# Performance work log

Hardware: AMD Instinct MI355X
Metric: run time of the kernel (lower is better)

## Reference

```python
import jax, jax.numpy as jnp
import numpy as np

B, T = 2, 512
E, NH, HD, V, P, L, KER, BLOCK = 768, 12, 64, 256, 4, 4, 16, 512
SCALE = HD ** -0.5


def _ln(x, g, b, eps=1e-5):
    m = jnp.mean(x, -1, keepdims=True)
    v = jnp.mean((x - m) ** 2, -1, keepdims=True)
    return (x - m) * jax.lax.rsqrt(v + eps) * g + b


def _rope_tables(n):
    inv = 1.0 / (10000.0 ** (jnp.arange(0, HD, 2, dtype=jnp.float32) / HD))
    f = jnp.arange(n, dtype=jnp.float32)[:, None] * inv[None, :]
    return jnp.cos(f), jnp.sin(f)


def _rope(x, cos, sin):
    # rotate over last two dims (positions, HD); split-half RoPE as in source
    h = x.shape[-1] // 2
    x1, x2 = x[..., :h], x[..., h:]
    return jnp.concatenate([x1 * cos - x2 * sin, x1 * sin + x2 * cos], axis=-1)


def _patch_attn(x, qkv_w, S):
    # x: [B,T,E]; sliding-window patch attention, step=1
    Bb, Tt, _ = x.shape
    q, k, v = jnp.split(x @ qkv_w, 3, axis=-1)
    heads = lambda t: t.reshape(Bb, Tt, NH, HD).transpose(0, 2, 1, 3)  # [B,NH,T,HD]
    q, k, v = heads(q), heads(k), heads(v)
    cos, sin = _rope_tables(Tt)
    q = _rope(q, cos, sin)
    k = _rope(k, cos, sin)
    # prefix: full causal attention over first S tokens
    sc = jnp.einsum('bnqh,bnkh->bnqk', q[:, :, :S], k[:, :, :S]) * SCALE
    mask = jnp.tril(jnp.ones((S, S), dtype=bool))
    sc = jnp.where(mask, sc, jnp.float32(-jnp.inf))
    out = jnp.einsum('bnqk,bnkh->bnqh', jax.nn.softmax(sc, axis=-1), v[:, :, :S])
    if Tt > S:
        # query t (t>=S) attends keys [t-S+1, t] (mask_sliding is all-ones for step=1)
        idx = jnp.arange(Tt - S)[:, None] + 1 + jnp.arange(S)[None, :]  # [T-S,S]
        kw = k[:, :, idx]  # [B,NH,T-S,S,HD]
        vw = v[:, :, idx]
        qs = q[:, :, S:]   # [B,NH,T-S,HD]
        sw = jnp.einsum('bnth,bntsh->bnts', qs, kw) * SCALE
        ow = jnp.einsum('bnts,bntsh->bnth', jax.nn.softmax(sw, axis=-1), vw)
        out = jnp.concatenate([out, ow], axis=2)
    return out.transpose(0, 2, 1, 3).reshape(Bb, Tt, NH * HD)


def _sa_block(x, ln0g, ln0b, ln1g, ln1b, qkv_w, proj_w, proj_b, w1, b1, w2, b2):
    # x: [B,T,P,V]; full (unmasked) attention over the P prediction slots
    Bb, Tt, Pp, _ = x.shape
    h = _ln(x, ln0g, ln0b)
    q, k, v = jnp.split(h @ qkv_w, 3, axis=-1)
    heads = lambda t: t.reshape(Bb, Tt, Pp, NH, HD).transpose(0, 1, 3, 2, 4)  # [B,T,NH,P,HD]
    q, k, v = heads(q), heads(k), heads(v)
    cos, sin = _rope_tables(Pp)
    q = _rope(q, cos, sin)
    k = _rope(k, cos, sin)
    sc = jnp.einsum('btnph,btnqh->btnpq', q, k) * SCALE
    o = jnp.einsum('btnpq,btnqh->btnph', jax.nn.softmax(sc, axis=-1), v)
    o = o.transpose(0, 1, 3, 2, 4).reshape(Bb, Tt, Pp, NH * HD)
    x = x + (o @ proj_w + proj_b)
    h2 = _ln(x, ln1g, ln1b)
    ff = jax.nn.gelu(h2 @ w1 + b1, approximate=False) @ w2 + b2
    return x + ff


def _forward(tokens, emb, blk_ln0_g, blk_ln0_b, blk_ln1_g, blk_ln1_b, blk_qkv_w,
             blk_ff_w1, blk_ff_b1, blk_ff_w2, blk_ff_b2, fin_ln_g, fin_ln_b,
             head_w, head_b, sa_ln0_g, sa_ln0_b, sa_ln1_g, sa_ln1_b, sa_qkv_w,
             sa_proj_w, sa_proj_b, sa_ff_w1, sa_ff_b1, sa_ff_w2, sa_ff_b2):
    x0 = emb[tokens]  # [B,T,E]
    x = x0
    for i in range(L):
        S = min(KER * 2 ** i, BLOCK)
        h = _ln(x, blk_ln0_g[i], blk_ln0_b[i])
        x = x + _patch_attn(h, blk_qkv_w[i], S)
        h2 = _ln(x, blk_ln1_g[i], blk_ln1_b[i])
        x = x + (jax.nn.gelu(h2 @ blk_ff_w1[i] + blk_ff_b1[i], approximate=False)
                 @ blk_ff_w2[i] + blk_ff_b2[i])
    x = x0 + x  # Golu: x = token_embedding(x); x = x + blocks(x)
    x = _ln(x, fin_ln_g, fin_ln_b)
    logits = (x @ head_w + head_b).reshape(B, T, P, V)
    logits = _sa_block(logits, sa_ln0_g, sa_ln0_b, sa_ln1_g, sa_ln1_b, sa_qkv_w,
                       sa_proj_w, sa_proj_b, sa_ff_w1, sa_ff_b1, sa_ff_w2, sa_ff_b2)
    return logits[:, :, 0, :]  # [B,T,V] (y is None path)


def setup_inputs() -> dict:
    key = jax.random.key(0)
    ks = jax.random.split(key, 12)
    w = lambda k, sh: jax.random.normal(k, sh, dtype=jnp.float32) * 0.02
    return {
        'tokens': jax.random.randint(ks[0], (B, T), 0, V),
        'emb': w(ks[1], (V, E)),
        'blk_ln0_g': jnp.ones((L, E), jnp.float32),
        'blk_ln0_b': jnp.zeros((L, E), jnp.float32),
        'blk_ln1_g': jnp.ones((L, E), jnp.float32),
        'blk_ln1_b': jnp.zeros((L, E), jnp.float32),
        'blk_qkv_w': w(ks[2], (L, E, 3 * E)),
        'blk_ff_w1': w(ks[3], (L, E, 4 * E)),
        'blk_ff_b1': jnp.zeros((L, 4 * E), jnp.float32),
        'blk_ff_w2': w(ks[4], (L, 4 * E, E)),
        'blk_ff_b2': jnp.zeros((L, E), jnp.float32),
        'fin_ln_g': jnp.ones((E,), jnp.float32),
        'fin_ln_b': jnp.zeros((E,), jnp.float32),
        'head_w': w(ks[5], (E, V * P)),
        'head_b': jnp.zeros((V * P,), jnp.float32),
        'sa_ln0_g': jnp.ones((V,), jnp.float32),
        'sa_ln0_b': jnp.zeros((V,), jnp.float32),
        'sa_ln1_g': jnp.ones((V,), jnp.float32),
        'sa_ln1_b': jnp.zeros((V,), jnp.float32),
        'sa_qkv_w': w(ks[6], (V, 3 * E)),
        'sa_proj_w': w(ks[7], (E, V)),
        'sa_proj_b': jnp.zeros((V,), jnp.float32),
        'sa_ff_w1': w(ks[8], (V, 4 * V)),
        'sa_ff_b1': jnp.zeros((4 * V,), jnp.float32),
        'sa_ff_w2': w(ks[9], (4 * V, V)),
        'sa_ff_b2': jnp.zeros((V,), jnp.float32),
    }


def reference(tokens, emb, blk_ln0_g, blk_ln0_b, blk_ln1_g, blk_ln1_b, blk_qkv_w,
              blk_ff_w1, blk_ff_b1, blk_ff_w2, blk_ff_b2, fin_ln_g, fin_ln_b,
              head_w, head_b, sa_ln0_g, sa_ln0_b, sa_ln1_g, sa_ln1_b, sa_qkv_w,
              sa_proj_w, sa_proj_b, sa_ff_w1, sa_ff_b1, sa_ff_w2, sa_ff_b2):
    return _forward(tokens, emb, blk_ln0_g, blk_ln0_b, blk_ln1_g, blk_ln1_b,
                    blk_qkv_w, blk_ff_w1, blk_ff_b1, blk_ff_w2, blk_ff_b2,
                    fin_ln_g, fin_ln_b, head_w, head_b, sa_ln0_g, sa_ln0_b,
                    sa_ln1_g, sa_ln1_b, sa_qkv_w, sa_proj_w, sa_proj_b,
                    sa_ff_w1, sa_ff_b1, sa_ff_w2, sa_ff_b2)
```

## Files before the change

kernel.cpp:

```cpp
#include <hip/hip_runtime.h>
#include <hip/hip_bf16.h>
#include <cstdint>
#include <cstddef>

#define BB    2
#define TSEQ  512
#define EDIM  768
#define NHEAD 12
#define HDIM  64
#define VDIM  256
#define PDIM  4
#define NROW  (BB*TSEQ)
#define NROW2 (BB*TSEQ*PDIM)

typedef __attribute__((ext_vector_type(8))) short short8;
typedef __attribute__((ext_vector_type(4))) short short4v;
typedef __attribute__((ext_vector_type(4))) float floatx4;

__device__ __forceinline__ float gelu_f(float v){
    return 0.5f * v * (1.0f + erff(v * 0.70710678118654752f));
}
__device__ __forceinline__ float b2f(short s){
    unsigned u = ((unsigned)(unsigned short)s) << 16;
    float f; __builtin_memcpy(&f, &u, 4); return f;
}
__device__ __forceinline__ short f2bs(float v){
    __hip_bfloat16 h = __float2bfloat16(v);
    short s; __builtin_memcpy(&s, &h, 2); return s;
}
__device__ __forceinline__ void gload16(const void* g, void* l){
    __builtin_amdgcn_global_load_lds((const __attribute__((address_space(1))) void*)g,
                                     (__attribute__((address_space(3))) void*)l, 16, 0, 0);
}

#define WAITN(n) asm volatile("s_waitcnt vmcnt(" #n ")" ::: "memory")
#define WAIT_STAGE(rem, full, half)                         \
    do{ if((rem) >= 2)      WAITN(full);                    \
        else if((rem) == 1) WAITN(half);                    \
        else                WAITN(0);                       \
        asm volatile("s_barrier" ::: "memory"); }while(0)

struct WD2 { const float* in; __hip_bfloat16* out; int K; int N; int nt; };
struct WDs { WD2 d[17]; };

__global__ __launch_bounds__(256) void wconv_all(WDs a)
{
    int id = blockIdx.x;
    int i = 0;
    while(i < 16 && id >= a.d[i].nt){ id -= a.d[i].nt; i++; }
    WD2 w = a.d[i];
    const int tx = w.N / 128;
    const int n0 = (id % tx) * 128, k0 = (id / tx) * 128;
    __shared__ short t[128*128];
    {
        const int c4 = (threadIdx.x & 31) * 4;
        const int r0 = threadIdx.x >> 5;
        #pragma unroll
        for(int half = 0; half < 2; half++){
            float4 v[8];
            #pragma unroll
            for(int it = 0; it < 8; it++){
                int r = r0 + it*8 + half*64;
                v[it] = *(const float4*)(w.in + (size_t)(k0 + r) * w.N + n0 + c4);
            }
            #pragma unroll
            for(int it = 0; it < 8; it++){
                int r = r0 + it*8 + half*64;
                int nswz = c4 ^ (((r >> 3) & 15) << 2);
                short4v o;
                o[0] = f2bs(v[it].x); o[1] = f2bs(v[it].y);
                o[2] = f2bs(v[it].z); o[3] = f2bs(v[it].w);
                *(short4v*)&t[r*128 + nswz] = o;
            }
        }
    }
    __syncthreads();
    {
        const int k8 = (threadIdx.x & 15) * 8;
        const int nr = threadIdx.x >> 4;
        const int swz = (k8 >> 3) << 2;
        #pragma unroll
        for(int pass = 0; pass < 8; pass++){
            int n = nr + pass*16;
            int nswz = n ^ swz;
            short8 o;
            #pragma unroll
            for(int j = 0; j < 8; j++) o[j] = t[(k8 + j)*128 + nswz];
            *(short8*)((short*)w.out + (size_t)(n0 + n) * w.K + k0 + k8) = o;
        }
    }
}

template<int ACT, int RESID, int OUTBF16, int ROPESA>
__global__ __launch_bounds__(256) void gemm128(
    const short* __restrict__ A, const short* __restrict__ Bt,
    const float* __restrict__ bias, const float* __restrict__ resid,
    void* __restrict__ Cout, const float* __restrict__ rc, const float* __restrict__ rs,
    int M, int N, int K)
{
    alignas(16) __shared__ short As[4*128*32];
    alignas(16) __shared__ short Bs[4*128*32];
    const int tid  = threadIdx.x;
    const int lane = tid & 63;
    const int wave = tid >> 6;
    const int bm = blockIdx.y * 128, bn = blockIdx.x * 128;
    const int wm = (wave >> 1) * 64, wn = (wave & 1) * 64;
    const int quad = lane >> 4, l16 = lane & 15;

    floatx4 acc[4][4];
    #pragma unroll
    for(int i = 0; i < 4; i++)
        #pragma unroll
        for(int j = 0; j < 4; j++)
            acc[i][j] = floatx4{0.f, 0.f, 0.f, 0.f};

    const int r  = tid >> 2;
    const int c8 = (tid & 3) * 8;
    const int ldsoff = (tid & 192) * 16;

    auto issue = [&](int k0, int cur){
        char* ab = (char*)As + cur*8192 + ldsoff;
        char* bb = (char*)Bs + cur*8192 + ldsoff;
        gload16(A  + (size_t)(bm + r     ) * K + k0 + c8, ab);
        gload16(A  + (size_t)(bm + r + 64) * K + k0 + c8, ab + 4096);
        gload16(Bt + (size_t)(bn + r     ) * K + k0 + c8, bb);
        gload16(Bt + (size_t)(bn + r + 64) * K + k0 + c8, bb + 4096);
    };

    const int niter = K >> 5;
    issue(0, 0); issue(32, 1); issue(64, 2);
    for(int it = 0; it < niter; it++){
        WAIT_STAGE(niter - 1 - it, 8, 4);
        if(it + 3 < niter) issue((it + 3) << 5, (it + 3) & 3);
        const short* Ab = As + (it & 3) * 4096;
        const short* Bb = Bs + (it & 3) * 4096;
        short8 af[4], bfr[4];
        #pragma unroll
        for(int i = 0; i < 4; i++){
            af[i]  = *(const short8*)&Ab[(wm + i*16 + l16)*32 + quad*8];
            bfr[i] = *(const short8*)&Bb[(wn + i*16 + l16)*32 + quad*8];
        }
        #pragma unroll
        for(int i = 0; i < 4; i++)
            #pragma unroll
            for(int j = 0; j < 4; j++)
                acc[i][j] = __builtin_amdgcn_mfma_f32_16x16x32_bf16(af[i], bfr[j], acc[i][j], 0, 0, 0);
    }

    float* Cf = (float*)Cout;
    __hip_bfloat16* Cb = (__hip_bfloat16*)Cout;

    if(ROPESA){
        const int hb = bn + wn;
        const int region = hb / 768;
        #pragma unroll
        for(int i = 0; i < 4; i++){
            #pragma unroll
            for(int rr = 0; rr < 4; rr++){
                int row = bm + wm + i*16 + quad*4 + rr;
                float a0 = acc[i][0][rr], a1 = acc[i][1][rr];
                float a2 = acc[i][2][rr], a3 = acc[i][3][rr];
                size_t rowb = (size_t)row * N + hb;
                if(region == 2){
                    Cb[rowb + l16]      = __float2bfloat16(a0);
                    Cb[rowb + 16 + l16] = __float2bfloat16(a1);
                    Cb[rowb + 32 + l16] = __float2bfloat16(a2);
                    Cb[rowb + 48 + l16] = __float2bfloat16(a3);
                }else{
                    int p = row & 3;
                    float c0 = rc[p*32 + l16],      s0 = rs[p*32 + l16];
                    float c1 = rc[p*32 + 16 + l16], s1 = rs[p*32 + 16 + l16];
                    Cb[rowb + l16]      = __float2bfloat16(a0*c0 - a2*s0);
                    Cb[rowb + 16 + l16] = __float2bfloat16(a1*c1 - a3*s1);
                    Cb[rowb + 32 + l16] = __float2bfloat16(a0*s0 + a2*c0);
                    Cb[rowb + 48 + l16] = __float2bfloat16(a1*s1 + a3*c1);
                }
            }
        }
        return;
    }

    #pragma unroll
    for(int i = 0; i < 4; i++){
        int row0 = bm + wm + i*16 + quad*4;
        #pragma unroll
        for(int j = 0; j < 4; j++){
            int col = bn + wn + j*16 + l16;
            float bv = bias ? bias[col] : 0.f;
            #pragma unroll
            for(int rr = 0; rr < 4; rr++){
                float v = acc[i][j][rr] + bv;
                if(ACT) v = gelu_f(v);
                if(RESID) v += resid[(size_t)(row0 + rr) * N + col];
                if(OUTBF16) Cb[(size_t)(row0 + rr) * N + col] = __float2bfloat16(v);
                else        Cf[(size_t)(row0 + rr) * N + col] = v;
            }
        }
    }
}

template<int EPI>
__global__ __launch_bounds__(256) void gemm64q(
    const short* __restrict__ A, const short* __restrict__ Bt,
    const float* __restrict__ bias, __hip_bfloat16* __restrict__ Cout,
    __hip_bfloat16* __restrict__ qrb, __hip_bfloat16* __restrict__ krb,
    __hip_bfloat16* __restrict__ vvb,
    const float* __restrict__ rc, const float* __restrict__ rs,
    int M, int N, int K)
{
    alignas(16) __shared__ short As[4*64*32];
    alignas(16) __shared__ short Bs[4*64*32];
    const int tid  = threadIdx.x;
    const int lane = tid & 63;
    const int wave = tid >> 6;
    const int bm = blockIdx.y * 64, bn = blockIdx.x * 64;
    const int wm = wave * 16;
    const int quad = lane >> 4, l16 = lane & 15;

    floatx4 acc[4];
    #pragma unroll
    for(int j = 0; j < 4; j++) acc[j] = floatx4{0.f, 0.f, 0.f, 0.f};

    const int r  = tid >> 2;
    const int c8 = (tid & 3) * 8;
    const int ldsoff = (tid & 192) * 16;

    auto issue = [&](int k0, int cur){
        char* ab = (char*)As + cur*4096 + ldsoff;
        char* bb = (char*)Bs + cur*4096 + ldsoff;
        gload16(A  + (size_t)(bm + r) * K + k0 + c8, ab);
        gload16(Bt + (size_t)(bn + r) * K + k0 + c8, bb);
    };

    const int niter = K >> 5;
    issue(0, 0); issue(32, 1); issue(64, 2);
    for(int it = 0; it < niter; it++){
        WAIT_STAGE(niter - 1 - it, 4, 2);
        if(it + 3 < niter) issue((it + 3) << 5, (it + 3) & 3);
        const short* Ab = As + (it & 3) * 2048;
        const short* Bb = Bs + (it & 3) * 2048;
        short8 af = *(const short8*)&Ab[(wm + l16)*32 + quad*8];
        short8 bfr[4];
        #pragma unroll
        for(int j = 0; j < 4; j++)
            bfr[j] = *(const short8*)&Bb[(j*16 + l16)*32 + quad*8];
        #pragma unroll
        for(int j = 0; j < 4; j++)
            acc[j] = __builtin_amdgcn_mfma_f32_16x16x32_bf16(af, bfr[j], acc[j], 0, 0, 0);
    }

    if(EPI == 2){
        const int region = bn / 768;
        const int h = (bn % 768) >> 6;
        #pragma unroll
        for(int rr = 0; rr < 4; rr++){
            int row = bm + wm + quad*4 + rr;
            int t = row & (TSEQ-1), b = row >> 9;
            float a0 = acc[0][rr], a1 = acc[1][rr];
            float a2 = acc[2][rr], a3 = acc[3][rr];
            size_t dbase = ((size_t)(b*NHEAD + h)*TSEQ + t)*HDIM;
            if(region == 2){
                vvb[dbase + l16]      = __float2bfloat16(a0);
                vvb[dbase + 16 + l16] = __float2bfloat16(a1);
                vvb[dbase + 32 + l16] = __float2bfloat16(a2);
                vvb[dbase + 48 + l16] = __float2bfloat16(a3);
            }else{
                float c0 = rc[t*32 + l16],      s0 = rs[t*32 + l16];
                float c1 = rc[t*32 + 16 + l16], s1 = rs[t*32 + 16 + l16];
                __hip_bfloat16* dst = (region == 0) ? qrb : krb;
                dst[dbase + l16]      = __float2bfloat16(a0*c0 - a2*s0);
                dst[dbase + 16 + l16] = __float2bfloat16(a1*c1 - a3*s1);
                dst[dbase + 32 + l16] = __float2bfloat16(a0*s0 + a2*c0);
                dst[dbase + 48 + l16] = __float2bfloat16(a1*s1 + a3*c1);
            }
        }
        return;
    }

    if(EPI == 3){
        const int region = bn / 768;
        #pragma unroll
        for(int rr = 0; rr < 4; rr++){
            int row = bm + wm + quad*4 + rr;
            float a0 = acc[0][rr], a1 = acc[1][rr];
            float a2 = acc[2][rr], a3 = acc[3][rr];
            size_t rowb = (size_t)row * N + bn;
            if(region == 2){
                Cout[rowb + l16]      = __float2bfloat16(a0);
                Cout[rowb + 16 + l16] = __float2bfloat16(a1);
                Cout[rowb + 32 + l16] = __float2bfloat16(a2);
                Cout[rowb + 48 + l16] = __float2bfloat16(a3);
            }else{
                int p = row & 3;
                float c0 = rc[p*32 + l16],      s0 = rs[p*32 + l16];
                float c1 = rc[p*32 + 16 + l16], s1 = rs[p*32 + 16 + l16];
                Cout[rowb + l16]      = __float2bfloat16(a0*c0 - a2*s0);
                Cout[rowb + 16 + l16] = __float2bfloat16(a1*c1 - a3*s1);
                Cout[rowb + 32 + l16] = __float2bfloat16(a0*s0 + a2*c0);
                Cout[rowb + 48 + l16] = __float2bfloat16(a1*s1 + a3*c1);
            }
        }
        return;
    }

    #pragma unroll
    for(int j = 0; j < 4; j++){
        int col = bn + j*16 + l16;
        float bv = bias ? bias[col] : 0.f;
        #pragma unroll
        for(int rr = 0; rr < 4; rr++){
            int row = bm + wm + quad*4 + rr;
            float v = acc[j][rr] + bv;
            v = gelu_f(v);
            Cout[(size_t)row * N + col] = __float2bfloat16(v);
        }
    }
}

template<int RESID, int OUTC>
__global__ __launch_bounds__(256) void gemm64t(
    const short* __restrict__ A, const short* __restrict__ Bt,
    const float* __restrict__ bias, const float* __restrict__ resid,
    float* __restrict__ Cf, float* __restrict__ outp, int M, int N, int K)
{
    alignas(16) __shared__ short As[4*64*32];
    alignas(16) __shared__ short Bs[4*64*32];
    const int tid  = threadIdx.x;
    const int lane = tid & 63;
    const int wave = tid >> 6;
    const int bm = blockIdx.y * 64, bn = blockIdx.x * 64;
    const int wm = (wave >> 1) * 32, wn = (wave & 1) * 32;
    const int quad = lane >> 4, l16 = lane & 15;

    floatx4 acc[2][2];
    #pragma unroll
    for(int i = 0; i < 2; i++)
        #pragma unroll
        for(int j = 0; j < 2; j++)
            acc[i][j] = floatx4{0.f, 0.f, 0.f, 0.f};

    const int r  = tid >> 2;
    const int c8 = (tid & 3) * 8;
    const int ldsoff = (tid & 192) * 16;

    auto issue = [&](int k0, int cur){
        char* ab = (char*)As + cur*4096 + ldsoff;
        char* bb = (char*)Bs + cur*4096 + ldsoff;
        gload16(A  + (size_t)(bm + r) * K + k0 + c8, ab);
        gload16(Bt + (size_t)(bn + r) * K + k0 + c8, bb);
    };

    const int niter = K >> 5;
    issue(0, 0); issue(32, 1); issue(64, 2);
    for(int it = 0; it < niter; it++){
        WAIT_STAGE(niter - 1 - it, 4, 2);
        if(it + 3 < niter) issue((it + 3) << 5, (it + 3) & 3);
        const short* Ab = As + (it & 3) * 2048;
        const short* Bb = Bs + (it & 3) * 2048;
        short8 af[2], bfr[2];
        #pragma unroll
        for(int i = 0; i < 2; i++){
            af[i]  = *(const short8*)&Ab[(wm + i*16 + l16)*32 + quad*8];
            bfr[i] = *(const short8*)&Bb[(wn + i*16 + l16)*32 + quad*8];
        }
        #pragma unroll
        for(int i = 0; i < 2; i++)
            #pragma unroll
            for(int j = 0; j < 2; j++)
                acc[i][j] = __builtin_amdgcn_mfma_f32_16x16x32_bf16(af[i], bfr[j], acc[i][j], 0, 0, 0);
    }

    #pragma unroll
    for(int i = 0; i < 2; i++){
        int row0 = bm + wm + i*16 + quad*4;
        #pragma unroll
        for(int j = 0; j < 2; j++){
            int col = bn + wn + j*16 + l16;
            float bv = bias ? bias[col] : 0.f;
            #pragma unroll
            for(int rr = 0; rr < 4; rr++){
                int row = row0 + rr;
                float v = acc[i][j][rr] + bv;
                if(RESID) v += resid[(size_t)row * N + col];
                Cf[(size_t)row * N + col] = v;
                if(OUTC && (row & 3) == 0)
                    outp[(size_t)(row >> 2) * N + col] = v;
            }
        }
    }
}

template<int D>
__global__ __launch_bounds__(256) void ln_wave(
    const float* __restrict__ in, const float* __restrict__ in2,
    const float* __restrict__ g, const float* __restrict__ bta,
    __hip_bfloat16* __restrict__ out)
{
    constexpr int NC = D / 256;
    const int row  = blockIdx.x * 4 + (threadIdx.x >> 6);
    const int lane = threadIdx.x & 63;
    const float* xr = in + (size_t)row * D;
    float4 v[NC];
    float sum = 0.f, sq = 0.f;
    #pragma unroll
    for(int j = 0; j < NC; j++){
        int d0 = (lane + 64*j) * 4;
        v[j] = *(const float4*)(xr + d0);
        if(in2){
            float4 u = *(const float4*)(in2 + (size_t)row * D + d0);
            v[j].x += u.x; v[j].y += u.y; v[j].z += u.z; v[j].w += u.w;
        }
        sum += v[j].x + v[j].y + v[j].z + v[j].w;
        sq  += v[j].x*v[j].x + v[j].y*v[j].y + v[j].z*v[j].z + v[j].w*v[j].w;
    }
    #pragma unroll
    for(int off = 32; off > 0; off >>= 1){
        sum += __shfl_xor(sum, off, 64);
        sq  += __shfl_xor(sq,  off, 64);
    }
    const float m    = sum / D;
    const float rstd = rsqrtf(fmaxf(sq / D - m*m, 0.f) + 1e-5f);
    #pragma unroll
    for(int j = 0; j < NC; j++){
        int d0 = (lane + 64*j) * 4;
        float4 gg = *(const float4*)(g + d0);
        float4 bb = *(const float4*)(bta + d0);
        short4v o;
        o[0] = f2bs((v[j].x - m) * rstd * gg.x + bb.x);
        o[1] = f2bs((v[j].y - m) * rstd * gg.y + bb.y);
        o[2] = f2bs((v[j].z - m) * rstd * gg.z + bb.z);
        o[3] = f2bs((v[j].w - m) * rstd * gg.w + bb.w);
        *(short4v*)((short*)out + (size_t)row * D + d0) = o;
    }
}

__global__ __launch_bounds__(256) void embed_rope(
    const int* __restrict__ tokens, const float* __restrict__ emb,
    float* __restrict__ x0, float* __restrict__ x,
    float* __restrict__ rc, float* __restrict__ rs)
{
    const int blk = blockIdx.x;
    if(blk < NROW){
        const int tok = tokens[blk];
        const float4* src = (const float4*)(emb + (size_t)tok * EDIM);
        float4* d0 = (float4*)(x0 + (size_t)blk * EDIM);
        float4* d1 = (float4*)(x  + (size_t)blk * EDIM);
        if(threadIdx.x < EDIM/4){
            float4 v = src[threadIdx.x]; d0[threadIdx.x] = v; d1[threadIdx.x] = v;
        }
        return;
    }
    int i = (blk - NROW) * 256 + threadIdx.x;
    int pos = i >> 5, d = i & 31;
    float inv = powf(10000.0f, -(float)(2*d) / 64.0f);
    float f = (float)pos * inv;
    rc[i] = cosf(f);
    rs[i] = sinf(f);
}

template<int S>
__global__ __launch_bounds__(256) void patch_attn16(
    const __hip_bfloat16* __restrict__ qr, const __hip_bfloat16* __restrict__ kr,
    const __hip_bfloat16* __restrict__ vv, float* __restrict__ x)
{
    constexpr int W = S + 15;
    alignas(16) __shared__ short Ks[W*64];
    alignas(16) __shared__ short Vs[W*64];
    __shared__ float qlds[16*64];
    __shared__ float pb[16*128];

    const int t0 = blockIdx.x * 16;
    const int h = blockIdx.y, b = blockIdx.z;
    const int tid = threadIdx.x;
    const int wv = tid >> 6, lane = tid & 63;
    const size_t headbase = ((size_t)(b*NHEAD + h)) * TSEQ;

    const int c = tid & 7;
    for(int r = tid >> 3; r < W; r += 32){
        int g = t0 - S + 1 + r;
        int gc = g < 0 ? 0 : g;
        int sc = (c ^ (r & 7)) * 8;
        *(short8*)&Ks[r*64 + sc] = *(const short8*)((const short*)kr + (headbase + gc)*64 + c*8);
        *(short8*)&Vs[r*64 + sc] = *(const short8*)((const short*)vv + (headbase + gc)*64 + c*8);
    }
    for(int i = tid; i < 16*64; i += 256)
        qlds[i] = __bfloat162float(qr[(headbase + t0 + (i >> 6))*64 + (i & 63)]);
    __syncthreads();

    #pragma unroll
    for(int qq = 0; qq < 4; qq++){
        const int ql = wv*4 + qq;
        const int t  = t0 + ql;
        const int r0 = (S >= 64) ? (ql + lane) : ((lane < S) ? (ql + lane) : 0);
        const int r1 = ql + lane + 64;
        float a0 = 0.f, a1 = 0.f;
        #pragma unroll
        for(int ch = 0; ch < 8; ch++){
            float4 qa = *(const float4*)&qlds[ql*64 + ch*8];
            float4 qb = *(const float4*)&qlds[ql*64 + ch*8 + 4];
            short8 k0 = *(const short8*)&Ks[r0*64 + ((ch ^ (r0 & 7))*8)];
            a0 += qa.x*b2f(k0[0]) + qa.y*b2f(k0[1]) + qa.z*b2f(k0[2]) + qa.w*b2f(k0[3])
                + qb.x*b2f(k0[4]) + qb.y*b2f(k0[5]) + qb.z*b2f(k0[6]) + qb.w*b2f(k0[7]);
            if(S == 128){
                short8 k1 = *(const short8*)&Ks[r1*64 + ((ch ^ (r1 & 7))*8)];
                a1 += qa.x*b2f(k1[0]) + qa.y*b2f(k1[1]) + qa.z*b2f(k1[2]) + qa.w*b2f(k1[3])
                    + qb.x*b2f(k1[4]) + qb.y*b2f(k1[5]) + qb.z*b2f(k1[6]) + qb.w*b2f(k1[7]);
            }
        }
        const int key0 = t - S + 1 + lane;
        const bool v0 = (lane < S) && (key0 >= 0);
        const bool v1 = (S == 128) && (key0 + 64 >= 0);
        float s0 = v0 ? a0 * 0.125f : -1e30f;
        float s1 = v1 ? a1 * 0.125f : -1e30f;
        float mx = fmaxf(s0, s1);
        #pragma unroll
        for(int off = 32; off > 0; off >>= 1) mx = fmaxf(mx, __shfl_xor(mx, off, 64));
        float p0 = v0 ? expf(s0 - mx) : 0.f;
        float p1 = v1 ? expf(s1 - mx) : 0.f;
        float sm = p0 + p1;
        #pragma unroll
        for(int off = 32; off > 0; off >>= 1) sm += __shfl_xor(sm, off, 64);
        const float inv = 1.f / sm;
        pb[ql*128 + lane] = p0 * inv;
        if(S == 128) pb[ql*128 + lane + 64] = p1 * inv;
    }

    const int d = lane;
    const int coff = d >> 3, dlo = d & 7;
    #pragma unroll
    for(int qq = 0; qq < 4; qq++){
        const int ql = wv*4 + qq;
        float o = 0.f;
        #pragma unroll 8
        for(int j = 0; j < S; j++){
            int r = ql + j;
            float p = pb[ql*128 + j];
            o += p * b2f(Vs[r*64 + ((coff ^ (r & 7))*8) + dlo]);
        }
        x[((size_t)(b*TSEQ) + t0 + ql) * EDIM + h*HDIM + d] += o;
    }
}

__global__ __launch_bounds__(256) void sa_attn(
    const __hip_bfloat16* __restrict__ qkv2, __hip_bfloat16* __restrict__ o)
{
    const int t = blockIdx.x, h = blockIdx.y, b = blockIdx.z;
    const int p = threadIdx.x >> 6, lane = threadIdx.x & 63;
    const int row0 = (b*TSEQ + t) * PDIM;
    const short* base = (const short*)qkv2 + (size_t)row0 * (3*EDIM);
    const int d = lane;
    float q = b2f(base[(size_t)p*(3*EDIM) + h*HDIM + d]);
    float sc[4];
    #pragma unroll
    for(int j = 0; j < 4; j++){
        float kj = b2f(base[(size_t)j*(3*EDIM) + EDIM + h*HDIM + d]);
        float v = q * kj;
        #pragma unroll
        for(int off = 32; off > 0; off >>= 1) v += __shfl_xor(v, off, 64);
        sc[j] = v * 0.125f;
    }
    float m = fmaxf(fmaxf(sc[0], sc[1]), fmaxf(sc[2], sc[3]));
    float e0 = expf(sc[0]-m), e1 = expf(sc[1]-m), e2 = expf(sc[2]-m), e3 = expf(sc[3]-m);
    float idn = 1.f / (e0 + e1 + e2 + e3);
    float ov = (e0 * b2f(base[0*(3*EDIM) + 2*EDIM + h*HDIM + d])
              + e1 * b2f(base[1*(3*EDIM) + 2*EDIM + h*HDIM + d])
              + e2 * b2f(base[2*(3*EDIM) + 2*EDIM + h*HDIM + d])
              + e3 * b2f(base[3*(3*EDIM) + 2*EDIM + h*HDIM + d])) * idn;
    o[(size_t)(row0 + p) * EDIM + h*HDIM + d] = __float2bfloat16(ov);
}

extern "C" void kernel_launch(void* const* d_in, const int* in_sizes, int n_in,
                              void* d_out, int out_size, void* d_ws, size_t ws_size,
                              hipStream_t stream)
{
    const int*   tokens    = (const int*)  d_in[0];
    const float* emb       = (const float*)d_in[1];
    const float* bl0g      = (const float*)d_in[2];
    const float* bl0b      = (const float*)d_in[3];
    const float* bl1g      = (const float*)d_in[4];
    const float* bl1b      = (const float*)d_in[5];
    const float* qkv_w     = (const float*)d_in[6];
    const float* ff_w1     = (const float*)d_in[7];
    const float* ff_b1     = (const float*)d_in[8];
    const float* ff_w2     = (const float*)d_in[9];
    const float* ff_b2     = (const float*)d_in[10];
    const float* fin_g     = (const float*)d_in[11];
    const float* fin_b     = (const float*)d_in[12];
    const float* head_w    = (const float*)d_in[13];
    const float* head_b    = (const float*)d_in[14];
    const float* sa_ln0_g  = (const float*)d_in[15];
    const float* sa_ln0_b  = (const float*)d_in[16];
    const float* sa_ln1_g  = (const float*)d_in[17];
    const float* sa_ln1_b  = (const float*)d_in[18];
    const float* sa_qkv_w  = (const float*)d_in[19];
    const float* sa_proj_w = (const float*)d_in[20];
    const float* sa_proj_b = (const float*)d_in[21];
    const float* sa_ff_w1  = (const float*)d_in[22];
    const float* sa_ff_b1  = (const float*)d_in[23];
    const float* sa_ff_w2  = (const float*)d_in[24];
    const float* sa_ff_b2  = (const float*)d_in[25];
    float* out = (float*)d_out;

    char* p = (char*)d_ws;
    auto alloc = [&](size_t bytes){ char* q = p; p += (bytes + 255) & ~(size_t)255; return q; };

    float* logits = (float*)alloc((size_t)NROW2*VDIM*4);
    float* ropec  = (float*)alloc(512*32*4);
    float* ropes  = (float*)alloc(512*32*4);
    __hip_bfloat16* wqkvT[4]; for(int i=0;i<4;i++) wqkvT[i] = (__hip_bfloat16*)alloc((size_t)768*2304*2);
    __hip_bfloat16* wff1T[4]; for(int i=0;i<4;i++) wff1T[i] = (__hip_bfloat16*)alloc((size_t)768*3072*2);
    __hip_bfloat16* wff2T[4]; for(int i=0;i<4;i++) wff2T[i] = (__hip_bfloat16*)alloc((size_t)3072*768*2);
    __hip_bfloat16* wheadT   = (__hip_bfloat16*)alloc((size_t)768*1024*2);
    __hip_bfloat16* wsaqkvT  = (__hip_bfloat16*)alloc((size_t)256*2304*2);
    __hip_bfloat16* wsaprojT = (__hip_bfloat16*)alloc((size_t)768*256*2);
    __hip_bfloat16* wsaff1T  = (__hip_bfloat16*)alloc((size_t)256*1024*2);
    __hip_bfloat16* wsaff2T  = (__hip_bfloat16*)alloc((size_t)1024*256*2);
    char* U = p;
    float* x0           = (float*)(U);
    float* x            = (float*)(U + 3145728);
    __hip_bfloat16* h   = (__hip_bfloat16*)(U + 6291456);
    __hip_bfloat16* ff1 = (__hip_bfloat16*)(U + 7864320);
    __hip_bfloat16* qrb = (__hip_bfloat16*)(U + 14155776);
    __hip_bfloat16* krb = (__hip_bfloat16*)(U + 15728640);
    __hip_bfloat16* vvb = (__hip_bfloat16*)(U + 17301504);
    __hip_bfloat16* h2    = (__hip_bfloat16*)(U);
    __hip_bfloat16* qkv2  = (__hip_bfloat16*)(U + 2097152);
    __hip_bfloat16* sa_o  = (__hip_bfloat16*)(U + 20971520);
    __hip_bfloat16* sa_f1 = (__hip_bfloat16*)(U + 27262976);

    embed_rope<<<NROW + 64, 256, 0, stream>>>(tokens, emb, x0, x, ropec, ropes);
    {
        WDs wds; int tot = 0, n = 0;
        auto add = [&](const float* in, __hip_bfloat16* o2, int K, int N){
            wds.d[n++] = WD2{in, o2, K, N, (N/128)*(K/128)};
            tot += (N/128)*(K/128);
        };
        for(int i=0;i<4;i++){
            add(qkv_w + (size_t)i*768*2304, wqkvT[i], 768, 2304);
            add(ff_w1 + (size_t)i*768*3072, wff1T[i], 768, 3072);
            add(ff_w2 + (size_t)i*3072*768, wff2T[i], 3072, 768);
        }
        add(head_w,    wheadT,   768, 1024);
        add(sa_qkv_w,  wsaqkvT,  256, 2304);
        add(sa_proj_w, wsaprojT, 768, 256);
        add(sa_ff_w1,  wsaff1T,  256, 1024);
        add(sa_ff_w2,  wsaff2T, 1024, 256);
        wconv_all<<<tot, 256, 0, stream>>>(wds);
    }

    for(int i = 0; i < 4; i++){
        ln_wave<EDIM><<<NROW/4, 256, 0, stream>>>(x, nullptr, bl0g + i*EDIM, bl0b + i*EDIM, h);
        gemm64q<2><<<dim3(36, 16), 256, 0, stream>>>(
            (const short*)h, (const short*)wqkvT[i], nullptr, nullptr,
            qrb, krb, vvb, ropec, ropes, NROW, 3*EDIM, EDIM);
        dim3 agrid(TSEQ/16, NHEAD, BB);
        if(i == 0)      patch_attn16<16><<<agrid, 256, 0, stream>>>(qrb, krb, vvb, x);
        else if(i == 1) patch_attn16<32><<<agrid, 256, 0, stream>>>(qrb, krb, vvb, x);
        else if(i == 2) patch_attn16<64><<<agrid, 256, 0, stream>>>(qrb, krb, vvb, x);
        else            patch_attn16<128><<<agrid, 256, 0, stream>>>(qrb, krb, vvb, x);
        ln_wave<EDIM><<<NROW/4, 256, 0, stream>>>(x, nullptr, bl1g + i*EDIM, bl1b + i*EDIM, h);
        gemm64q<1><<<dim3(48, 16), 256, 0, stream>>>(
            (const short*)h, (const short*)wff1T[i], ff_b1 + (size_t)i*4*EDIM, ff1,
            nullptr, nullptr, nullptr, nullptr, nullptr, NROW, 4*EDIM, EDIM);
        gemm64t<1,0><<<dim3(12, 16), 256, 0, stream>>>(
            (const short*)ff1, (const short*)wff2T[i], ff_b2 + (size_t)i*EDIM, x, x, nullptr,
            NROW, EDIM, 4*EDIM);
    }

    ln_wave<EDIM><<<NROW/4, 256, 0, stream>>>(x, x0, fin_g, fin_b, h);
    gemm64t<0,0><<<dim3(16, 16), 256, 0, stream>>>(
        (const short*)h, (const short*)wheadT, head_b, nullptr, logits, nullptr,
        NROW, PDIM*VDIM, EDIM);

    ln_wave<VDIM><<<NROW2/4, 256, 0, stream>>>(logits, nullptr, sa_ln0_g, sa_ln0_b, h2);
    gemm64q<3><<<dim3(36, 64), 256, 0, stream>>>(
        (const short*)h2, (const short*)wsaqkvT, nullptr, qkv2,
        nullptr, nullptr, nullptr, ropec, ropes, NROW2, 3*EDIM, VDIM);
    sa_attn<<<dim3(TSEQ, NHEAD, BB), 256, 0, stream>>>(qkv2, sa_o);
    gemm64t<1,0><<<dim3(4, 64), 256, 0, stream>>>(
        (const short*)sa_o, (const short*)wsaprojT, sa_proj_b, logits, logits, nullptr,
        NROW2, VDIM, EDIM);
    ln_wave<VDIM><<<NROW2/4, 256, 0, stream>>>(logits, nullptr, sa_ln1_g, sa_ln1_b, h2);
    gemm64q<1><<<dim3(16, 64), 256, 0, stream>>>(
        (const short*)h2, (const short*)wsaff1T, sa_ff_b1, sa_f1,
        nullptr, nullptr, nullptr, nullptr, nullptr, NROW2, 4*VDIM, VDIM);
    gemm64t<1,1><<<dim3(4, 64), 256, 0, stream>>>(
        (const short*)sa_f1, (const short*)wsaff2T, sa_ff_b2, logits, logits, out,
        NROW2, VDIM, 4*VDIM);
}
```

Measured before the change: 667.1 us.

## Replace 64x64 fp32-output GEMM with 32x64 two-wave kernel and 8-stage pipeline

Replaces the 64x64-tile, 4-wave gemm64t with gemm32t, which uses a 32x64 tile, two waves (each owning 16 rows across all 64 columns) and an 8-deep global-to-LDS prefetch ring in place of 4. The smaller tile doubles the grid for the narrow-N GEMMs (FF2, head, SA proj, SA FF2), aiming to fill more CUs. The deeper prefetch is meant to hide memory latency for the long-K FF2. In exchange, B tiles are reloaded by twice as many blocks and each wave does less MFMA work per LDS read. The unused gemm128 kernel is also deleted.

```diff
diff --git a/kernel.cpp b/kernel.cpp
--- a/kernel.cpp
+++ b/kernel.cpp
@@ -37,6 +37,15 @@
 #define WAIT_STAGE(rem, full, half)                         \
     do{ if((rem) >= 2)      WAITN(full);                    \
         else if((rem) == 1) WAITN(half);                    \
+        else                WAITN(0);                       \
+        asm volatile("s_barrier" ::: "memory"); }while(0)
+#define WAIT_STAGE8(rem)                                    \
+    do{ if((rem) >= 6)      WAITN(18);                      \
+        else if((rem) == 5) WAITN(15);                      \
+        else if((rem) == 4) WAITN(12);                      \
+        else if((rem) == 3) WAITN(9);                       \
+        else if((rem) == 2) WAITN(6);                       \
+        else if((rem) == 1) WAITN(3);                       \
         else                WAITN(0);                       \
         asm volatile("s_barrier" ::: "memory"); }while(0)
 
@@ -87,114 +96,6 @@
             #pragma unroll
             for(int j = 0; j < 8; j++) o[j] = t[(k8 + j)*128 + nswz];
             *(short8*)((short*)w.out + (size_t)(n0 + n) * w.K + k0 + k8) = o;
-        }
-    }
-}
-
-template<int ACT, int RESID, int OUTBF16, int ROPESA>
-__global__ __launch_bounds__(256) void gemm128(
-    const short* __restrict__ A, const short* __restrict__ Bt,
-    const float* __restrict__ bias, const float* __restrict__ resid,
-    void* __restrict__ Cout, const float* __restrict__ rc, const float* __restrict__ rs,
-    int M, int N, int K)
-{
-    alignas(16) __shared__ short As[4*128*32];
-    alignas(16) __shared__ short Bs[4*128*32];
-    const int tid  = threadIdx.x;
-    const int lane = tid & 63;
-    const int wave = tid >> 6;
-    const int bm = blockIdx.y * 128, bn = blockIdx.x * 128;
-    const int wm = (wave >> 1) * 64, wn = (wave & 1) * 64;
-    const int quad = lane >> 4, l16 = lane & 15;
-
-    floatx4 acc[4][4];
-    #pragma unroll
-    for(int i = 0; i < 4; i++)
-        #pragma unroll
-        for(int j = 0; j < 4; j++)
-            acc[i][j] = floatx4{0.f, 0.f, 0.f, 0.f};
-
-    const int r  = tid >> 2;
-    const int c8 = (tid & 3) * 8;
-    const int ldsoff = (tid & 192) * 16;
-
-    auto issue = [&](int k0, int cur){
-        char* ab = (char*)As + cur*8192 + ldsoff;
-        char* bb = (char*)Bs + cur*8192 + ldsoff;
-        gload16(A  + (size_t)(bm + r     ) * K + k0 + c8, ab);
-        gload16(A  + (size_t)(bm + r + 64) * K + k0 + c8, ab + 4096);
-        gload16(Bt + (size_t)(bn + r     ) * K + k0 + c8, bb);
-        gload16(Bt + (size_t)(bn + r + 64) * K + k0 + c8, bb + 4096);
-    };
-
-    const int niter = K >> 5;
-    issue(0, 0); issue(32, 1); issue(64, 2);
-    for(int it = 0; it < niter; it++){
-        WAIT_STAGE(niter - 1 - it, 8, 4);
-        if(it + 3 < niter) issue((it + 3) << 5, (it + 3) & 3);
-        const short* Ab = As + (it & 3) * 4096;
-        const short* Bb = Bs + (it & 3) * 4096;
-        short8 af[4], bfr[4];
-        #pragma unroll
-        for(int i = 0; i < 4; i++){
-            af[i]  = *(const short8*)&Ab[(wm + i*16 + l16)*32 + quad*8];
-            bfr[i] = *(const short8*)&Bb[(wn + i*16 + l16)*32 + quad*8];
-        }
-        #pragma unroll
-        for(int i = 0; i < 4; i++)
-            #pragma unroll
-            for(int j = 0; j < 4; j++)
-                acc[i][j] = __builtin_amdgcn_mfma_f32_16x16x32_bf16(af[i], bfr[j], acc[i][j], 0, 0, 0);
-    }
-
-    float* Cf = (float*)Cout;
-    __hip_bfloat16* Cb = (__hip_bfloat16*)Cout;
-
-    if(ROPESA){
-        const int hb = bn + wn;
-        const int region = hb / 768;
-        #pragma unroll
-        for(int i = 0; i < 4; i++){
-            #pragma unroll
-            for(int rr = 0; rr < 4; rr++){
-                int row = bm + wm + i*16 + quad*4 + rr;
-                float a0 = acc[i][0][rr], a1 = acc[i][1][rr];
-                float a2 = acc[i][2][rr], a3 = acc[i][3][rr];
-                size_t rowb = (size_t)row * N + hb;
-                if(region == 2){
-                    Cb[rowb + l16]      = __float2bfloat16(a0);
-                    Cb[rowb + 16 + l16] = __float2bfloat16(a1);
-                    Cb[rowb + 32 + l16] = __float2bfloat16(a2);
-                    Cb[rowb + 48 + l16] = __float2bfloat16(a3);
-                }else{
-                    int p = row & 3;
-                    float c0 = rc[p*32 + l16],      s0 = rs[p*32 + l16];
-                    float c1 = rc[p*32 + 16 + l16], s1 = rs[p*32 + 16 + l16];
-                    Cb[rowb + l16]      = __float2bfloat16(a0*c0 - a2*s0);
-                    Cb[rowb + 16 + l16] = __float2bfloat16(a1*c1 - a3*s1);
-                    Cb[rowb + 32 + l16] = __float2bfloat16(a0*s0 + a2*c0);
-                    Cb[rowb + 48 + l16] = __float2bfloat16(a1*s1 + a3*c1);
-                }
-            }
-        }
-        return;
-    }
-
-    #pragma unroll
-    for(int i = 0; i < 4; i++){
-        int row0 = bm + wm + i*16 + quad*4;
-        #pragma unroll
-        for(int j = 0; j < 4; j++){
-            int col = bn + wn + j*16 + l16;
-            float bv = bias ? bias[col] : 0.f;
-            #pragma unroll
-            for(int rr = 0; rr < 4; rr++){
-                float v = acc[i][j][rr] + bv;
-                if(ACT) v = gelu_f(v);
-                if(RESID) v += resid[(size_t)(row0 + rr) * N + col];
-                if(OUTBF16) Cb[(size_t)(row0 + rr) * N + col] = __float2bfloat16(v);
-                else        Cf[(size_t)(row0 + rr) * N + col] = v;
-            }
         }
     }
 }
@@ -318,74 +219,66 @@
 }
 
 template<int RESID, int OUTC>
-__global__ __launch_bounds__(256) void gemm64t(
+__global__ __launch_bounds__(128) void gemm32t(
     const short* __restrict__ A, const short* __restrict__ Bt,
     const float* __restrict__ bias, const float* __restrict__ resid,
     float* __restrict__ Cf, float* __restrict__ outp, int M, int N, int K)
 {
-    alignas(16) __shared__ short As[4*64*32];
-    alignas(16) __shared__ short Bs[4*64*32];
+    alignas(16) __shared__ short As[8*32*32];
+    alignas(16) __shared__ short Bs[8*64*32];
     const int tid  = threadIdx.x;
     const int lane = tid & 63;
     const int wave = tid >> 6;
-    const int bm = blockIdx.y * 64, bn = blockIdx.x * 64;
-    const int wm = (wave >> 1) * 32, wn = (wave & 1) * 32;
+    const int bm = blockIdx.y * 32, bn = blockIdx.x * 64;
+    const int wm = wave * 16;
     const int quad = lane >> 4, l16 = lane & 15;
 
-    floatx4 acc[2][2];
-    #pragma unroll
-    for(int i = 0; i < 2; i++)
-        #pragma unroll
-        for(int j = 0; j < 2; j++)
-            acc[i][j] = floatx4{0.f, 0.f, 0.f, 0.f};
+    floatx4 acc[4];
+    #pragma unroll
+    for(int j = 0; j < 4; j++) acc[j] = floatx4{0.f, 0.f, 0.f, 0.f};
 
     const int r  = tid >> 2;
     const int c8 = (tid & 3) * 8;
-    const int ldsoff = (tid & 192) * 16;
+    const int ldsoff = (tid & 64) * 16;
 
     auto issue = [&](int k0, int cur){
-        char* ab = (char*)As + cur*4096 + ldsoff;
+        char* ab = (char*)As + cur*2048 + ldsoff;
         char* bb = (char*)Bs + cur*4096 + ldsoff;
-        gload16(A  + (size_t)(bm + r) * K + k0 + c8, ab);
-        gload16(Bt + (size_t)(bn + r) * K + k0 + c8, bb);
+        gload16(A  + (size_t)(bm + r)      * K + k0 + c8, ab);
+        gload16(Bt + (size_t)(bn + r)      * K + k0 + c8, bb);
+        gload16(Bt + (size_t)(bn + r + 32) * K + k0 + c8, bb + 2048);
     };
 
     const int niter = K >> 5;
-    issue(0, 0); issue(32, 1); issue(64, 2);
+    issue(0, 0); issue(32, 1); issue(64, 2); issue(96, 3);
+    issue(128, 4); issue(160, 5); issue(192, 6);
     for(int it = 0; it < niter; it++){
-        WAIT_STAGE(niter - 1 - it, 4, 2);
-        if(it + 3 < niter) issue((it + 3) << 5, (it + 3) & 3);
-        const short* Ab = As + (it & 3) * 2048;
-        const short* Bb = Bs + (it & 3) * 2048;
-        short8 af[2], bfr[2];
-        #pragma unroll
-        for(int i = 0; i < 2; i++){
-            af[i]  = *(const short8*)&Ab[(wm + i*16 + l16)*32 + quad*8];
-            bfr[i] = *(const short8*)&Bb[(wn + i*16 + l16)*32 + quad*8];
-        }
-        #pragma unroll
-        for(int i = 0; i < 2; i++)
-            #pragma unroll
-            for(int j = 0; j < 2; j++)
-                acc[i][j] = __builtin_amdgcn_mfma_f32_16x16x32_bf16(af[i], bfr[j], acc[i][j], 0, 0, 0);
-    }
-
-    #pragma unroll
-    for(int i = 0; i < 2; i++){
-        int row0 = bm + wm + i*16 + quad*4;
-        #pragma unroll
-        for(int j = 0; j < 2; j++){
-            int col = bn + wn + j*16 + l16;
-            float bv = bias ? bias[col] : 0.f;
-            #pragma unroll
-            for(int rr = 0; rr < 4; rr++){
-                int row = row0 + rr;
-                float v = acc[i][j][rr] + bv;
-                if(RESID) v += resid[(size_t)row * N + col];
-                Cf[(size_t)row * N + col] = v;
-                if(OUTC && (row & 3) == 0)
-                    outp[(size_t)(row >> 2) * N + col] = v;
-            }
+        WAIT_STAGE8(niter - 1 - it);
+        if(it + 7 < niter) issue((it + 7) << 5, (it + 7) & 7);
+        const short* Ab = As + (it & 7) * 1024;
+        const short* Bb = Bs + (it & 7) * 2048;
+        short8 af = *(const short8*)&Ab[(wm + l16)*32 + quad*8];
+        short8 bfr[4];
+        #pragma unroll
+        for(int j = 0; j < 4; j++)
+            bfr[j] = *(const short8*)&Bb[(j*16 + l16)*32 + quad*8];
+        #pragma unroll
+        for(int j = 0; j < 4; j++)
+            acc[j] = __builtin_amdgcn_mfma_f32_16x16x32_bf16(af, bfr[j], acc[j], 0, 0, 0);
+    }
+
+    #pragma unroll
+    for(int j = 0; j < 4; j++){
+        int col = bn + j*16 + l16;
+        float bv = bias ? bias[col] : 0.f;
+        #pragma unroll
+        for(int rr = 0; rr < 4; rr++){
+            int row = bm + wm + quad*4 + rr;
+            float v = acc[j][rr] + bv;
+            if(RESID) v += resid[(size_t)row * N + col];
+            Cf[(size_t)row * N + col] = v;
+            if(OUTC && (row & 3) == 0)
+                outp[(size_t)(row >> 2) * N + col] = v;
         }
     }
 }
@@ -662,13 +555,13 @@
         gemm64q<1><<<dim3(48, 16), 256, 0, stream>>>(
             (const short*)h, (const short*)wff1T[i], ff_b1 + (size_t)i*4*EDIM, ff1,
             nullptr, nullptr, nullptr, nullptr, nullptr, NROW, 4*EDIM, EDIM);
-        gemm64t<1,0><<<dim3(12, 16), 256, 0, stream>>>(
+        gemm32t<1,0><<<dim3(12, 32), 128, 0, stream>>>(
             (const short*)ff1, (const short*)wff2T[i], ff_b2 + (size_t)i*EDIM, x, x, nullptr,
             NROW, EDIM, 4*EDIM);
     }
 
     ln_wave<EDIM><<<NROW/4, 256, 0, stream>>>(x, x0, fin_g, fin_b, h);
-    gemm64t<0,0><<<dim3(16, 16), 256, 0, stream>>>(
+    gemm32t<0,0><<<dim3(16, 32), 128, 0, stream>>>(
         (const short*)h, (const short*)wheadT, head_b, nullptr, logits, nullptr,
         NROW, PDIM*VDIM, EDIM);
 
@@ -677,14 +570,14 @@
         (const short*)h2, (const short*)wsaqkvT, nullptr, qkv2,
         nullptr, nullptr, nullptr, ropec, ropes, NROW2, 3*EDIM, VDIM);
     sa_attn<<<dim3(TSEQ, NHEAD, BB), 256, 0, stream>>>(qkv2, sa_o);
-    gemm64t<1,0><<<dim3(4, 64), 256, 0, stream>>>(
+    gemm32t<1,0><<<dim3(4, 128), 128, 0, stream>>>(
         (const short*)sa_o, (const short*)wsaprojT, sa_proj_b, logits, logits, nullptr,
         NROW2, VDIM, EDIM);
     ln_wave<VDIM><<<NROW2/4, 256, 0, stream>>>(logits, nullptr, sa_ln1_g, sa_ln1_b, h2);
     gemm64q<1><<<dim3(16, 64), 256, 0, stream>>>(
         (const short*)h2, (const short*)wsaff1T, sa_ff_b1, sa_f1,
         nullptr, nullptr, nullptr, nullptr, nullptr, NROW2, 4*VDIM, VDIM);
-    gemm64t<1,1><<<dim3(4, 64), 256, 0, stream>>>(
+    gemm32t<1,1><<<dim3(4, 128), 128, 0, stream>>>(
         (const short*)sa_f1, (const short*)wsaff2T, sa_ff_b2, logits, logits, out,
         NROW2, VDIM, 4*VDIM);
 }
```

After: 685.7 us. 2.8% more time.
